# Kernel optimization log

Hardware: AMD Instinct MI355X
Metric: run time of the kernel (lower is better)

The kernel has to match this reference:

```python
import jax, jax.numpy as jnp
import numpy as np

SIGMA = 2.0
B, F, N = 4, 64, 4096


def setup_inputs() -> dict:
    key = jax.random.key(0)
    emb_in = jax.random.normal(key, (B, F, N), dtype=jnp.float32)
    adj_in = jnp.zeros((B, N, N), dtype=jnp.float32)  # unused by the module, kept for interface fidelity
    return {"adj_in": adj_in, "emb_in": emb_in}


def reference(adj_in, emb_in):
    # torch .std() is over all elements with Bessel's correction (ddof=1)
    std = jnp.std(emb_in, ddof=1)
    coord = emb_in / std  # [B, F, N]
    fmap = coord.shape[1]
    # mean_f (a-b)^2 = (|a|^2 + |b|^2 - 2 a.b) / F  -- GEMM trick, avoids [B,F,N,N]
    sq = jnp.sum(coord * coord, axis=1)              # [B, N]
    inner = jnp.einsum('bfn,bfm->bnm', coord, coord)  # [B, N, N]
    d2 = (sq[:, :, None] + sq[:, None, :] - 2.0 * inner) / fmap
    d2 = jnp.maximum(d2, 0.0)  # guard tiny negatives from cancellation
    return jnp.exp(-d2 / SIGMA)
```

## Files before the change

### kernel.cpp

```cpp
#include <hip/hip_runtime.h>
#include <hip/hip_bf16.h>

namespace {

constexpr int kB = 4, kF = 64, kN = 4096;
constexpr int kM = kB * kF * kN;

typedef __attribute__((ext_vector_type(8))) short bf16x8;
typedef __attribute__((ext_vector_type(4))) float f32x4;

__device__ __forceinline__ void wave_red2(float& s, float& q) {
#pragma unroll
  for (int o = 32; o > 0; o >>= 1) {
    s += __shfl_down(s, o, 64);
    q += __shfl_down(q, o, 64);
  }
}

__global__ void k_reduce1(const float* __restrict__ emb, float* __restrict__ part) {
  int t = blockIdx.x * blockDim.x + threadIdx.x;
  float4 v = reinterpret_cast<const float4*>(emb)[t];
  float s = v.x + v.y + v.z + v.w;
  float q = v.x * v.x + v.y * v.y + v.z * v.z + v.w * v.w;
  wave_red2(s, q);
  __shared__ float ls[4], lq[4];
  int lane = threadIdx.x & 63, w = threadIdx.x >> 6;
  if (lane == 0) { ls[w] = s; lq[w] = q; }
  __syncthreads();
  if (threadIdx.x == 0) {
    s = ls[0] + ls[1] + ls[2] + ls[3];
    q = lq[0] + lq[1] + lq[2] + lq[3];
    part[blockIdx.x] = s;
    part[1024 + blockIdx.x] = q;
  }
}

__global__ __launch_bounds__(256) void k_convert(const float* __restrict__ emb,
                                                 const float* __restrict__ part,
                                                 unsigned short* __restrict__ coordT,
                                                 float* __restrict__ sq) {
  int t = threadIdx.x;
  float s = part[t] + part[t + 256] + part[t + 512] + part[t + 768];
  float q = part[1024 + t] + part[1280 + t] + part[1536 + t] + part[1792 + t];
  wave_red2(s, q);
  __shared__ float ls[4], lq[4];
  __shared__ float s_inv;
  int lane = t & 63, w = t >> 6;
  if (lane == 0) { ls[w] = s; lq[w] = q; }
  __syncthreads();
  if (t == 0) {
    s = ls[0] + ls[1] + ls[2] + ls[3];
    q = lq[0] + lq[1] + lq[2] + lq[3];
    float mean = s / (float)kM;
    float var = (q - s * mean) / (float)(kM - 1);
    s_inv = 1.0f / sqrtf(var);
  }
  __syncthreads();
  float inv_std = s_inv;

  int nl = t & 63, fq = t >> 6;
  int g = blockIdx.x * 64 + nl;
  int b = g >> 12, n = g & 4095;
  const float* src = emb + ((size_t)b * kF + fq * 16) * kN + n;
  alignas(16) unsigned short loc[16];
  float acc = 0.f;
#pragma unroll
  for (int f = 0; f < 16; f++) {
    float v = src[(size_t)f * kN] * inv_std;
    union { __hip_bfloat16 h; unsigned short u; } cv;
    cv.h = __float2bfloat16(v);
    loc[f] = cv.u;
    float vf = __bfloat162float(cv.h);
    acc += vf * vf;
  }
  bf16x8* dst = reinterpret_cast<bf16x8*>(coordT + (size_t)g * kF + fq * 16);
  dst[0] = reinterpret_cast<const bf16x8*>(loc)[0];
  dst[1] = reinterpret_cast<const bf16x8*>(loc)[1];

  __shared__ float pacc[4][64];
  pacc[fq][nl] = acc;
  __syncthreads();
  if (fq == 0) sq[g] = pacc[0][nl] + pacc[1][nl] + pacc[2][nl] + pacc[3][nl];
}

__global__ __launch_bounds__(256, 2) void k_gemm_exp(const unsigned short* __restrict__ coordT,
                                                     const float* __restrict__ sq,
                                                     float* __restrict__ out) {
  constexpr int kPitch = 260;
  __shared__ float lds[64 * kPitch];

  int b = blockIdx.z;
  int wid = threadIdx.x >> 6;
  int lane = threadIdx.x & 63;
  int lhi = lane >> 4, llo = lane & 15;
  int y0 = blockIdx.y * 64;
  int x0 = blockIdx.x * 256;
  int xw = x0 + wid * 64;
  const unsigned short* base = coordT + (size_t)b * kN * kF;

  bf16x8 af[4][2], bfr[4][2];
#pragma unroll
  for (int m = 0; m < 4; m++) {
    const unsigned short* p = base + (size_t)(xw + m * 16 + llo) * kF + lhi * 8;
    af[m][0] = *reinterpret_cast<const bf16x8*>(p);
    af[m][1] = *reinterpret_cast<const bf16x8*>(p + 32);
  }
#pragma unroll
  for (int n = 0; n < 4; n++) {
    const unsigned short* p = base + (size_t)(y0 + n * 16 + llo) * kF + lhi * 8;
    bfr[n][0] = *reinterpret_cast<const bf16x8*>(p);
    bfr[n][1] = *reinterpret_cast<const bf16x8*>(p + 32);
  }

  f32x4 acc[4][4] = {};
#pragma unroll
  for (int kk = 0; kk < 2; kk++)
#pragma unroll
    for (int m = 0; m < 4; m++)
#pragma unroll
      for (int n = 0; n < 4; n++)
        acc[m][n] = __builtin_amdgcn_mfma_f32_16x16x32_bf16(af[m][kk], bfr[n][kk], acc[m][n], 0, 0, 0);

  const float* sqb = sq + (size_t)b * kN;
  float si[4][4];
#pragma unroll
  for (int m = 0; m < 4; m++) {
    f32x4 tv = *reinterpret_cast<const f32x4*>(&sqb[xw + m * 16 + lhi * 4]);
    si[m][0] = tv[0]; si[m][1] = tv[1]; si[m][2] = tv[2]; si[m][3] = tv[3];
  }
  float sj[4];
#pragma unroll
  for (int n = 0; n < 4; n++) sj[n] = sqb[y0 + n * 16 + llo];

  constexpr float kC = -0.011271055f;
#pragma unroll
  for (int m = 0; m < 4; m++) {
#pragma unroll
    for (int n = 0; n < 4; n++) {
      f32x4 wv;
#pragma unroll
      for (int r = 0; r < 4; r++) {
        float raw = si[m][r] + sj[n] - 2.0f * acc[m][n][r];
        raw = fmaxf(raw, 0.0f);
        wv[r] = __builtin_amdgcn_exp2f(raw * kC);
      }
      int yloc = n * 16 + llo;
      int xloc = wid * 64 + m * 16 + lhi * 4;
      *reinterpret_cast<f32x4*>(&lds[yloc * kPitch + xloc]) = wv;
    }
  }
  __syncthreads();

  float* ob = out + (size_t)b * kN * kN + (size_t)y0 * kN + x0;
#pragma unroll
  for (int p = 0; p < 16; p++) {
    int yloc = wid * 16 + p;
    f32x4 v = *reinterpret_cast<const f32x4*>(&lds[yloc * kPitch + lane * 4]);
    __builtin_nontemporal_store(v, reinterpret_cast<f32x4*>(ob + (size_t)yloc * kN + lane * 4));
  }
}

}

extern "C" void kernel_launch(void* const* d_in, const int* in_sizes, int n_in,
                              void* d_out, int out_size, void* d_ws, size_t ws_size,
                              hipStream_t stream) {
  const float* emb = (const float*)d_in[1];
  float* out = (float*)d_out;

  float* part = (float*)d_ws;
  unsigned short* coordT = (unsigned short*)((char*)d_ws + 16384);
  float* sq = (float*)((char*)d_ws + 16384 + (size_t)kB * kN * kF * sizeof(unsigned short));

  k_reduce1<<<1024, 256, 0, stream>>>(emb, part);
  k_convert<<<(kB * kN) / 64, 256, 0, stream>>>(emb, part, coordT, sq);
  dim3 grid(kN / 256, kN / 64, kB);
  k_gemm_exp<<<grid, 256, 0, stream>>>(coordT, sq, out);
}
```

Before: 70.50 us.

## Fold exp scaling into coords, seed MFMA accumulators, drop LDS staging

Pre-scales the coordinates by sqrt(log2e/(F*sigma)) and stores -0.5*|x|^2, so the exp2 argument comes straight out of the MFMA accumulator. The accumulators are seeded with the norm terms, which removes the per-element epilogue arithmetic. The LDS transpose and its barrier are removed and results go directly from registers as 16-byte stores. Occupancy is raised to 3 blocks per CU. The price is less coalesced global writes (16-byte chunks spread across rows) and the loss of nontemporal stores on a store-bound 256 MB output.

Result: slower. 74.60 us (+5.8%).

```diff
diff --git a/kernel.cpp b/kernel.cpp
--- a/kernel.cpp
+++ b/kernel.cpp
@@ -38,13 +38,13 @@
 __global__ __launch_bounds__(256) void k_convert(const float* __restrict__ emb,
                                                  const float* __restrict__ part,
                                                  unsigned short* __restrict__ coordT,
-                                                 float* __restrict__ sq) {
+                                                 float* __restrict__ sqp) {
   int t = threadIdx.x;
   float s = part[t] + part[t + 256] + part[t + 512] + part[t + 768];
   float q = part[1024 + t] + part[1280 + t] + part[1536 + t] + part[1792 + t];
   wave_red2(s, q);
   __shared__ float ls[4], lq[4];
-  __shared__ float s_inv;
+  __shared__ float s_scale;
   int lane = t & 63, w = t >> 6;
   if (lane == 0) { ls[w] = s; lq[w] = q; }
   __syncthreads();
@@ -53,10 +53,10 @@
     q = lq[0] + lq[1] + lq[2] + lq[3];
     float mean = s / (float)kM;
     float var = (q - s * mean) / (float)(kM - 1);
-    s_inv = 1.0f / sqrtf(var);
+    s_scale = 0.15014030f / sqrtf(var);
   }
   __syncthreads();
-  float inv_std = s_inv;
+  float scale = s_scale;
 
   int nl = t & 63, fq = t >> 6;
   int g = blockIdx.x * 64 + nl;
@@ -66,7 +66,7 @@
   float acc = 0.f;
 #pragma unroll
   for (int f = 0; f < 16; f++) {
-    float v = src[(size_t)f * kN] * inv_std;
+    float v = src[(size_t)f * kN] * scale;
     union { __hip_bfloat16 h; unsigned short u; } cv;
     cv.h = __float2bfloat16(v);
     loc[f] = cv.u;
@@ -80,15 +80,12 @@
   __shared__ float pacc[4][64];
   pacc[fq][nl] = acc;
   __syncthreads();
-  if (fq == 0) sq[g] = pacc[0][nl] + pacc[1][nl] + pacc[2][nl] + pacc[3][nl];
+  if (fq == 0) sqp[g] = -0.5f * (pacc[0][nl] + pacc[1][nl] + pacc[2][nl] + pacc[3][nl]);
 }
 
-__global__ __launch_bounds__(256, 2) void k_gemm_exp(const unsigned short* __restrict__ coordT,
-                                                     const float* __restrict__ sq,
+__global__ __launch_bounds__(256, 3) void k_gemm_exp(const unsigned short* __restrict__ coordT,
+                                                     const float* __restrict__ sqp,
                                                      float* __restrict__ out) {
-  constexpr int kPitch = 260;
-  __shared__ float lds[64 * kPitch];
-
   int b = blockIdx.z;
   int wid = threadIdx.x >> 6;
   int lane = threadIdx.x & 63;
@@ -97,6 +94,17 @@
   int x0 = blockIdx.x * 256;
   int xw = x0 + wid * 64;
   const unsigned short* base = coordT + (size_t)b * kN * kF;
+  const float* sqb = sqp + (size_t)b * kN;
+
+  float si[4][4];
+#pragma unroll
+  for (int m = 0; m < 4; m++) {
+    f32x4 tv = *reinterpret_cast<const f32x4*>(&sqb[xw + m * 16 + lhi * 4]);
+    si[m][0] = tv[0]; si[m][1] = tv[1]; si[m][2] = tv[2]; si[m][3] = tv[3];
+  }
+  float sj[4];
+#pragma unroll
+  for (int n = 0; n < 4; n++) sj[n] = sqb[y0 + n * 16 + llo];
 
   bf16x8 af[4][2], bfr[4][2];
 #pragma unroll
@@ -112,7 +120,15 @@
     bfr[n][1] = *reinterpret_cast<const bf16x8*>(p + 32);
   }
 
-  f32x4 acc[4][4] = {};
+  f32x4 acc[4][4];
+#pragma unroll
+  for (int m = 0; m < 4; m++)
+#pragma unroll
+    for (int n = 0; n < 4; n++)
+#pragma unroll
+      for (int r = 0; r < 4; r++)
+        acc[m][n][r] = si[m][r] + sj[n];
+
 #pragma unroll
   for (int kk = 0; kk < 2; kk++)
 #pragma unroll
@@ -121,42 +137,18 @@
       for (int n = 0; n < 4; n++)
         acc[m][n] = __builtin_amdgcn_mfma_f32_16x16x32_bf16(af[m][kk], bfr[n][kk], acc[m][n], 0, 0, 0);
 
-  const float* sqb = sq + (size_t)b * kN;
-  float si[4][4];
+  float* ob = out + (size_t)b * kN * kN;
 #pragma unroll
-  for (int m = 0; m < 4; m++) {
-    f32x4 tv = *reinterpret_cast<const f32x4*>(&sqb[xw + m * 16 + lhi * 4]);
-    si[m][0] = tv[0]; si[m][1] = tv[1]; si[m][2] = tv[2]; si[m][3] = tv[3];
-  }
-  float sj[4];
+  for (int n = 0; n < 4; n++) {
+    float* rp = ob + (size_t)(y0 + n * 16 + llo) * kN + xw + (lhi << 2);
 #pragma unroll
-  for (int n = 0; n < 4; n++) sj[n] = sqb[y0 + n * 16 + llo];
-
-  constexpr float kC = -0.011271055f;
-#pragma unroll
-  for (int m = 0; m < 4; m++) {
-#pragma unroll
-    for (int n = 0; n < 4; n++) {
+    for (int m = 0; m < 4; m++) {
       f32x4 wv;
 #pragma unroll
-      for (int r = 0; r < 4; r++) {
-        float raw = si[m][r] + sj[n] - 2.0f * acc[m][n][r];
-        raw = fmaxf(raw, 0.0f);
-        wv[r] = __builtin_amdgcn_exp2f(raw * kC);
-      }
-      int yloc = n * 16 + llo;
-      int xloc = wid * 64 + m * 16 + lhi * 4;
-      *reinterpret_cast<f32x4*>(&lds[yloc * kPitch + xloc]) = wv;
+      for (int r = 0; r < 4; r++)
+        wv[r] = __builtin_amdgcn_exp2f(fminf(acc[m][n][r], 0.0f));
+      *reinterpret_cast<f32x4*>(rp + m * 16) = wv;
     }
-  }
-  __syncthreads();
-
-  float* ob = out + (size_t)b * kN * kN + (size_t)y0 * kN + x0;
-#pragma unroll
-  for (int p = 0; p < 16; p++) {
-    int yloc = wid * 16 + p;
-    f32x4 v = *reinterpret_cast<const f32x4*>(&lds[yloc * kPitch + lane * 4]);
-    __builtin_nontemporal_store(v, reinterpret_cast<f32x4*>(ob + (size_t)yloc * kN + lane * 4));
   }
 }
 
@@ -170,10 +162,10 @@
 
   float* part = (float*)d_ws;
   unsigned short* coordT = (unsigned short*)((char*)d_ws + 16384);
-  float* sq = (float*)((char*)d_ws + 16384 + (size_t)kB * kN * kF * sizeof(unsigned short));
+  float* sqp = (float*)((char*)d_ws + 16384 + (size_t)kB * kN * kF * sizeof(unsigned short));
 
   k_reduce1<<<1024, 256, 0, stream>>>(emb, part);
-  k_convert<<<(kB * kN) / 64, 256, 0, stream>>>(emb, part, coordT, sq);
+  k_convert<<<(kB * kN) / 64, 256, 0, stream>>>(emb, part, coordT, sqp);
   dim3 grid(kN / 256, kN / 64, kB);
-  k_gemm_exp<<<grid, 256, 0, stream>>>(coordT, sq, out);
+  k_gemm_exp<<<grid, 256, 0, stream>>>(coordT, sqp, out);
 }
```
